# Kernel tuning notes

Measured on AMD Instinct MI355X. Metric: run time of the kernel, lower is better.

The kernel has to match this reference:

```python
import jax, jax.numpy as jnp
import numpy as np

N_NODES, N_EDGES, N_GRAPHS = 20000, 320000, 8
IN_CH, OUT_CH = 16, 64


def gat_conv(x, src, dst, W, a_src, a_dst, bias, heads, ch, concat):
    # PyG-style GATConv: linear -> per-edge attention logits -> edge softmax over dst -> scatter-sum
    n = x.shape[0]
    h = (x @ W).reshape(n, heads, ch)                      # [N,H,C]
    alpha_src = jnp.einsum('nhc,hc->nh', h, a_src)          # [N,H]
    alpha_dst = jnp.einsum('nhc,hc->nh', h, a_dst)
    e = jax.nn.leaky_relu(alpha_src[src] + alpha_dst[dst], 0.2)  # [E,H]
    emax = jax.ops.segment_max(e, dst, num_segments=n)      # safe: self-loops guarantee coverage
    ee = jnp.exp(e - emax[dst])
    denom = jax.ops.segment_sum(ee, dst, num_segments=n)
    alpha = ee / denom[dst]                                 # [E,H]
    msg = h[src] * alpha[:, :, None]                        # [E,H,C]
    out = jax.ops.segment_sum(msg, dst, num_segments=n)     # [N,H,C]
    out = out.reshape(n, heads * ch) if concat else out.mean(axis=1)
    return out + bias


def setup_inputs() -> dict:
    key = jax.random.key(0)
    ks = jax.random.split(key, 32)
    d = {}
    d['x'] = jax.random.normal(ks[0], (N_NODES, IN_CH), dtype=jnp.float32)
    d['edge_index'] = jax.random.randint(ks[1], (2, N_EDGES), 0, N_NODES)
    d['function_idx'] = jax.random.randint(ks[2], (8000,), 0, N_NODES)
    d['flag'] = jnp.sort(jax.random.randint(ks[3], (8000,), 0, N_GRAPHS))
    d['decision_var_idxes'] = jax.random.randint(ks[4], (N_GRAPHS,), 0, N_NODES)
    s = 0.1
    # conv1: in 16 -> 8 heads x 8
    d['W1'] = jax.random.normal(ks[5], (IN_CH, 64)) * s
    d['a_src1'] = jax.random.normal(ks[6], (8, 8)) * s
    d['a_dst1'] = jax.random.normal(ks[7], (8, 8)) * s
    d['b1'] = jnp.zeros((64,), jnp.float32)
    # conv2, conv3: 64 -> 8 heads x 8
    d['W2'] = jax.random.normal(ks[8], (64, 64)) * s
    d['a_src2'] = jax.random.normal(ks[9], (8, 8)) * s
    d['a_dst2'] = jax.random.normal(ks[10], (8, 8)) * s
    d['b2'] = jnp.zeros((64,), jnp.float32)
    d['W3'] = jax.random.normal(ks[11], (64, 64)) * s
    d['a_src3'] = jax.random.normal(ks[12], (8, 8)) * s
    d['a_dst3'] = jax.random.normal(ks[13], (8, 8)) * s
    d['b3'] = jnp.zeros((64,), jnp.float32)
    # conv4: 64 -> 4 heads x 64, concat=False (mean over heads)
    d['W4'] = jax.random.normal(ks[14], (64, 4 * OUT_CH)) * s
    d['a_src4'] = jax.random.normal(ks[15], (4, OUT_CH)) * s
    d['a_dst4'] = jax.random.normal(ks[16], (4, OUT_CH)) * s
    d['b4'] = jnp.zeros((OUT_CH,), jnp.float32)
    d['Wp'] = jax.random.normal(ks[17], (OUT_CH, OUT_CH)) * s
    d['Wt'] = jax.random.normal(ks[18], (OUT_CH, OUT_CH)) * s
    d['Wo'] = jax.random.normal(ks[19], (2 * OUT_CH, 1)) * s
    d['bo'] = jnp.zeros((1,), jnp.float32)
    return d


def reference(x, edge_index, function_idx, flag, decision_var_idxes,
              W1, a_src1, a_dst1, b1, W2, a_src2, a_dst2, b2,
              W3, a_src3, a_dst3, b3, W4, a_src4, a_dst4, b4,
              Wp, Wt, Wo, bo):
    n = x.shape[0]
    loops = jnp.arange(n)
    src = jnp.concatenate([edge_index[0], loops])
    dst = jnp.concatenate([edge_index[1], loops])
    h = jax.nn.elu(gat_conv(x, src, dst, W1, a_src1, a_dst1, b1, 8, 8, True))
    h = jax.nn.elu(gat_conv(h, src, dst, W2, a_src2, a_dst2, b2, 8, 8, True))
    h = jax.nn.elu(gat_conv(h, src, dst, W3, a_src3, a_dst3, b3, 8, 8, True))
    h = jax.nn.elu(gat_conv(h, src, dst, W4, a_src4, a_dst4, b4, 4, OUT_CH, False))
    # per-graph sum-pool over function nodes
    fp = jax.ops.segment_sum(h[function_idx], flag, num_segments=N_GRAPHS)  # [B,64]
    fp = fp @ Wp
    tgt = h[decision_var_idxes] @ Wt                                        # [B,64]
    z = jax.nn.elu(jnp.concatenate([fp, tgt], axis=1))                      # [B,128]
    return z @ Wo + bo                                                      # [B,1]
```

## Files before the change

kernel.cpp:

```cpp
#include <hip/hip_runtime.h>
#include <hip/hip_bf16.h>
#include <math.h>

typedef __hip_bfloat16 bf16;
typedef unsigned short u16;
typedef __attribute__((ext_vector_type(8))) short bf16x8;
typedef __attribute__((ext_vector_type(4))) float f32x4;

#define DEG_CAP 96

__device__ __forceinline__ float b2f(bf16 v){ return __bfloat162float(v); }
__device__ __forceinline__ u16 f2bu(float f){
  bf16 h = __float2bfloat16(f);
  return *reinterpret_cast<u16*>(&h);
}
__device__ __forceinline__ float bu2f(u16 u){
  bf16 h = *reinterpret_cast<bf16*>(&u);
  return __bfloat162float(h);
}
__device__ __forceinline__ float eluf(float x){ return x > 0.f ? x : __expf(x) - 1.f; }
__device__ __forceinline__ float lrelu(float x){ return x > 0.f ? x : 0.2f * x; }
__device__ __forceinline__ float ldr(const void* p, int i, int f){
  return f ? ((const float*)p)[i] : b2f(((const bf16*)p)[i]);
}

#define DPP_F(x, ctrl) __int_as_float(__builtin_amdgcn_update_dpp(0, __float_as_int(x), (ctrl), 0xF, 0xF, true))
__device__ __forceinline__ float dpp_max8(float x){
  x = fmaxf(x, DPP_F(x, 0xB1));
  x = fmaxf(x, DPP_F(x, 0x4E));
  x = fmaxf(x, DPP_F(x, 0x141));
  return x;
}
__device__ __forceinline__ float dpp_sum8(float x){
  x += DPP_F(x, 0xB1);
  x += DPP_F(x, 0x4E);
  x += DPP_F(x, 0x141);
  return x;
}
__device__ __forceinline__ float dpp_max16(float x){
  x = fmaxf(x, DPP_F(x, 0xB1));
  x = fmaxf(x, DPP_F(x, 0x4E));
  x = fmaxf(x, DPP_F(x, 0x141));
  x = fmaxf(x, DPP_F(x, 0x140));
  return x;
}
__device__ __forceinline__ float dpp_sum16(float x){
  x += DPP_F(x, 0xB1);
  x += DPP_F(x, 0x4E);
  x += DPP_F(x, 0x141);
  x += DPP_F(x, 0x140);
  return x;
}
__device__ __forceinline__ float dpp_addx1(float x){ return x + DPP_F(x, 0xB1); }

__global__ void detect_zero_k(const u16* __restrict__ x, int nprobe, int* __restrict__ flag,
                              int* __restrict__ fill, float* __restrict__ fp,
                              int* __restrict__ ticket, int n){
  int i = blockIdx.x * 256 + threadIdx.x;
  if (i < n) fill[i] = 0;
  if (i < 512) fp[i] = 0.f;
  if (i == 0) *ticket = 0;
  if (blockIdx.x == 0){
    __shared__ int bad_s;
    if (threadIdx.x == 0) bad_s = 0;
    __syncthreads();
    int bad = 0;
    for (int k = threadIdx.x; k < nprobe; k += 256){
      int ex = (x[k] >> 7) & 0xFF;
      if (ex >= 0xC6) bad = 1;
    }
    if (bad) atomicOr(&bad_s, 1);
    __syncthreads();
    if (threadIdx.x == 0) *flag = bad_s;
  }
}

struct ConvDesc {
  const void* src[17];
  int off[18];
};

__global__ void prep_k(ConvDesc d, float* __restrict__ out, const int* __restrict__ flag,
                       int total, const int* __restrict__ ei, int E, int n,
                       int* __restrict__ fill, int* __restrict__ esrc,
                       const void* __restrict__ W4r, const void* __restrict__ as4r,
                       const void* __restrict__ ad4r, float* __restrict__ avs,
                       float* __restrict__ avd, u16* __restrict__ wzh,
                       u16* __restrict__ wzl,
                       const void* __restrict__ x_raw, const void* __restrict__ W1r,
                       const void* __restrict__ as1r, const void* __restrict__ ad1r,
                       u16* __restrict__ hl1, float* __restrict__ asrc1,
                       float* __restrict__ adst1,
                       int CB, int EB){
  __shared__ float wl1[16 * 64];
  __shared__ float xr1[16][20];
  int b = blockIdx.x;
  int f = *flag;
  int t = threadIdx.x;
  if (b < CB){
    int i = b * 256 + t;
    if (i >= total) return;
    int a = 0;
    while (i >= d.off[a + 1]) ++a;
    out[i] = ldr(d.src[a], i - d.off[a], f);
  } else if (b < CB + EB){
    int e = (b - CB) * 256 + t;
    if (e >= E + n) return;
    int s, dd;
    if (e < E){ s = ei[e]; dd = ei[E + e]; } else { s = e - E; dd = s; }
    int pos = atomicAdd(&fill[dd], 1);
    if (pos < DEG_CAP) esrc[dd * DEG_CAP + pos] = s;
  } else if (b < CB + EB + 64){
    int pb = b - CB - EB;
    int g = pb * 256 + t;
    int r = g >> 6, c = g & 63;
    int h = r >> 6, k = r & 63;
    float ww = 0.25f * ldr(W4r, k * 256 + h * 64 + c, f);
    u16 hi = f2bu(ww);
    wzh[c * 256 + r] = hi;
    wzl[c * 256 + r] = f2bu(ww - bu2f(hi));
    if (pb == 0){
      int th = t >> 6, tk = t & 63;
      float s1 = 0.f, s2 = 0.f;
      for (int cc = 0; cc < 64; ++cc){
        float w = ldr(W4r, tk * 256 + th * 64 + cc, f);
        s1 += w * ldr(as4r, th * 64 + cc, f);
        s2 += w * ldr(ad4r, th * 64 + cc, f);
      }
      avs[t] = s1;
      avd[t] = s2;
    }
  } else {
    int lb = b - CB - EB - 64;
    int base = lb * 16;
    int lane = t & 63, wv = t >> 6;
    int node = wv * 4 + (lane >> 4);
    int jj = lane & 15;
    for (int i = t; i < 1024; i += 256) wl1[i] = ldr(W1r, i, f);
    for (int q = t; q < 64; q += 256){
      int nd = q >> 2, k4 = q & 3;
      float4 v = make_float4(0.f, 0.f, 0.f, 0.f);
      if (base + nd < n){
        if (f){
          v = *(const float4*)((const float*)x_raw + (base + nd) * 16 + k4 * 4);
        } else {
          ushort4 v4 = *(const ushort4*)((const u16*)x_raw + (base + nd) * 16 + k4 * 4);
          v = make_float4(bu2f(v4.x), bu2f(v4.y), bu2f(v4.z), bu2f(v4.w));
        }
      }
      *(float4*)(&xr1[nd][k4 * 4]) = v;
    }
    __syncthreads();
    float ax = 0.f, ay = 0.f, az = 0.f, aw = 0.f;
#pragma unroll
    for (int k4 = 0; k4 < 4; ++k4){
      float4 xv = *(const float4*)(&xr1[node][k4 * 4]);
      float4 w0 = ((const float4*)wl1)[(k4 * 4 + 0) * 16 + jj];
      float4 w1 = ((const float4*)wl1)[(k4 * 4 + 1) * 16 + jj];
      float4 w2 = ((const float4*)wl1)[(k4 * 4 + 2) * 16 + jj];
      float4 w3 = ((const float4*)wl1)[(k4 * 4 + 3) * 16 + jj];
      ax += xv.x * w0.x + xv.y * w1.x + xv.z * w2.x + xv.w * w3.x;
      ay += xv.x * w0.y + xv.y * w1.y + xv.z * w2.y + xv.w * w3.y;
      az += xv.x * w0.z + xv.y * w1.z + xv.z * w2.z + xv.w * w3.z;
      aw += xv.x * w0.w + xv.y * w1.w + xv.z * w2.w + xv.w * w3.w;
    }
    int gn = base + node;
    if (gn < n){
      ushort4 o4;
      o4.x = f2bu(ax); o4.y = f2bu(ay); o4.z = f2bu(az); o4.w = f2bu(aw);
      ((ushort4*)(hl1 + gn * 64))[jj] = o4;
    }
    float as_[4], ad_[4];
#pragma unroll
    for (int c = 0; c < 4; ++c){
      as_[c] = ldr(as1r, 4 * jj + c, f);
      ad_[c] = ldr(ad1r, 4 * jj + c, f);
    }
    float s1 = ax * as_[0] + ay * as_[1] + az * as_[2] + aw * as_[3];
    float s2 = ax * ad_[0] + ay * ad_[1] + az * ad_[2] + aw * ad_[3];
    s1 = dpp_addx1(s1);
    s2 = dpp_addx1(s2);
    if (gn < n){
      int hh = jj >> 1;
      if ((jj & 1) == 0) asrc1[gn * 8 + hh] = s1;
      else               adst1[gn * 8 + hh] = s2;
    }
  }
}

template<int NEXT>
__global__ void agg8f_k(const u16* __restrict__ hlin, const float* __restrict__ asrc,
                        const float* __restrict__ adst, const int* __restrict__ cnts,
                        const int* __restrict__ esrc, const float* __restrict__ bias,
                        const float* __restrict__ Wn,
                        const float* __restrict__ a_srcn, const float* __restrict__ a_dstn,
                        const float* __restrict__ avs, const float* __restrict__ avd,
                        u16* __restrict__ hout, u16* __restrict__ ylin,
                        float* __restrict__ asrco, float* __restrict__ adsto, int n){
  __shared__ float wl[NEXT == 1 ? 4096 : 1];
  __shared__ float os[4][64];
  if (NEXT == 1){
    for (int q = threadIdx.x; q < 1024; q += 256)
      ((float4*)wl)[q] = ((const float4*)Wn)[q];
    __syncthreads();
  }
  int node = (blockIdx.x * blockDim.x + threadIdx.x) >> 6;
  if (node >= n) return;
  int lane = threadIdx.x & 63;
  int wv = (threadIdx.x >> 6) & 3;
  int h = lane >> 3;
  int j = lane & 7;
  int cp = lane & 15;
  int q  = lane >> 4;
  int hh = cp >> 1;
  int wlane0 = hh * 8 + q;
  int wlane1 = hh * 8 + 4 + q;
  int sclane = hh * 8;
  int beg = node * DEG_CAP;
  int cnt = cnts[node]; if (cnt > DEG_CAP) cnt = DEG_CAP;
  int end = beg + cnt;
  float ad = adst[node * 8 + h];

  float m = -INFINITY, swp = 0.f;
  float4 acc = make_float4(0.f, 0.f, 0.f, 0.f);

  int   s_cur = 0; float l_cur = -INFINITY;
  if (beg + j < end){ s_cur = esrc[beg + j]; l_cur = lrelu(asrc[s_cur * 8 + h] + ad); }
  int s0c = __shfl(s_cur, q), s1c = __shfl(s_cur, 4 + q);
  ushort4 hv0 = *(const ushort4*)(hlin + s0c * 64 + cp * 4);
  ushort4 hv1 = *(const ushort4*)(hlin + s1c * 64 + cp * 4);
  int   s_nx = 0; float l_nx = -INFINITY;
  if (beg + 8 + j < end){ s_nx = esrc[beg + 8 + j]; l_nx = lrelu(asrc[s_nx * 8 + h] + ad); }

  for (int b0 = beg; b0 < end; b0 += 8){
    int s0n = __shfl(s_nx, q), s1n = __shfl(s_nx, 4 + q);
    ushort4 hv0n = *(const ushort4*)(hlin + s0n * 64 + cp * 4);
    ushort4 hv1n = *(const ushort4*)(hlin + s1n * 64 + cp * 4);
    int p2 = b0 + 16 + j;
    int s_n2 = 0; float l_n2 = -INFINITY;
    if (p2 < end){ s_n2 = esrc[p2]; l_n2 = lrelu(asrc[s_n2 * 8 + h] + ad); }
    float bm = dpp_max8(l_cur);
    float mn = fmaxf(m, bm);
    if (!__all(bm <= m)){
      float scale = __expf(m - mn);
      swp *= scale;
      float scale_g = __shfl(scale, sclane);
      acc.x *= scale_g; acc.y *= scale_g; acc.z *= scale_g; acc.w *= scale_g;
      m = mn;
    }
    float w = (b0 + j < end) ? __expf(l_cur - m) : 0.f;
    swp += w;
    float w0 = __shfl(w, wlane0);
    float w1 = __shfl(w, wlane1);
    acc.x += bu2f(hv0.x) * w0 + bu2f(hv1.x) * w1;
    acc.y += bu2f(hv0.y) * w0 + bu2f(hv1.y) * w1;
    acc.z += bu2f(hv0.z) * w0 + bu2f(hv1.z) * w1;
    acc.w += bu2f(hv0.w) * w0 + bu2f(hv1.w) * w1;
    hv0 = hv0n; hv1 = hv1n;
    l_cur = l_nx;
    s_nx = s_n2; l_nx = l_n2;
  }
  acc.x += __shfl_xor(acc.x, 16); acc.x += __shfl_xor(acc.x, 32);
  acc.y += __shfl_xor(acc.y, 16); acc.y += __shfl_xor(acc.y, 32);
  acc.z += __shfl_xor(acc.z, 16); acc.z += __shfl_xor(acc.z, 32);
  acc.w += __shfl_xor(acc.w, 16); acc.w += __shfl_xor(acc.w, 32);
  swp = dpp_sum8(swp);
  float sw_g = __shfl(swp, sclane);
  float4 bv = ((const float4*)bias)[cp];
  float4 o4;
  o4.x = eluf(acc.x / sw_g + bv.x);
  o4.y = eluf(acc.y / sw_g + bv.y);
  o4.z = eluf(acc.z / sw_g + bv.z);
  o4.w = eluf(acc.w / sw_g + bv.w);

  if (NEXT == 1){
    if (lane < 16) *(float4*)(&os[wv][cp * 4]) = o4;
    int jj = lane & 15, kk = lane >> 4;
    const float4* osr = (const float4*)(&os[wv][kk * 16]);
    float ax = 0.f, ay = 0.f, az = 0.f, aw = 0.f;
#pragma unroll
    for (int k4 = 0; k4 < 4; ++k4){
      float4 xv = osr[k4];
      float4 w0 = ((const float4*)wl)[(kk * 16 + k4 * 4 + 0) * 16 + jj];
      float4 w1 = ((const float4*)wl)[(kk * 16 + k4 * 4 + 1) * 16 + jj];
      float4 w2 = ((const float4*)wl)[(kk * 16 + k4 * 4 + 2) * 16 + jj];
      float4 w3 = ((const float4*)wl)[(kk * 16 + k4 * 4 + 3) * 16 + jj];
      ax += xv.x * w0.x + xv.y * w1.x + xv.z * w2.x + xv.w * w3.x;
      ay += xv.x * w0.y + xv.y * w1.y + xv.z * w2.y + xv.w * w3.y;
      az += xv.x * w0.z + xv.y * w1.z + xv.z * w2.z + xv.w * w3.z;
      aw += xv.x * w0.w + xv.y * w1.w + xv.z * w2.w + xv.w * w3.w;
    }
    ax += __shfl_xor(ax, 16); ax += __shfl_xor(ax, 32);
    ay += __shfl_xor(ay, 16); ay += __shfl_xor(ay, 32);
    az += __shfl_xor(az, 16); az += __shfl_xor(az, 32);
    aw += __shfl_xor(aw, 16); aw += __shfl_xor(aw, 32);
    if (lane < 16){
      ushort4 y4;
      y4.x = f2bu(ax); y4.y = f2bu(ay); y4.z = f2bu(az); y4.w = f2bu(aw);
      ((ushort4*)(ylin + node * 64))[jj] = y4;
      float4 as = *(const float4*)(a_srcn + 4 * jj);
      float4 adn = *(const float4*)(a_dstn + 4 * jj);
      float s1 = ax * as.x + ay * as.y + az * as.z + aw * as.w;
      float s2 = ax * adn.x + ay * adn.y + az * adn.z + aw * adn.w;
      s1 = dpp_addx1(s1);
      s2 = dpp_addx1(s2);
      int nh = jj >> 1;
      if ((jj & 1) == 0) asrco[node * 8 + nh] = s1;
      else               adsto[node * 8 + nh] = s2;
    }
  } else {
    if (lane < 16){
      ushort4 ho;
      ho.x = f2bu(o4.x); ho.y = f2bu(o4.y); ho.z = f2bu(o4.z); ho.w = f2bu(o4.w);
      ((ushort4*)(hout + node * 64))[cp] = ho;
      *(float4*)(&os[wv][cp * 4]) = o4;
    }
    int t8 = lane & 7, ah = (lane >> 3) & 3, sd = lane >> 5;
    const float* av = sd ? avd : avs;
    const float4* op = (const float4*)(&os[wv][t8 * 8]);
    const float4* ap = (const float4*)(av + ah * 64 + t8 * 8);
    float4 o0 = op[0], o1 = op[1];
    float4 a0 = ap[0], a1 = ap[1];
    float part = o0.x * a0.x + o0.y * a0.y + o0.z * a0.z + o0.w * a0.w
               + o1.x * a1.x + o1.y * a1.y + o1.z * a1.z + o1.w * a1.w;
    part = dpp_sum8(part);
    if (t8 == 0){
      if (sd == 0) asrco[node * 4 + ah] = part;
      else         adsto[node * 4 + ah] = part;
    }
  }
}

__global__ void aggz_k(const u16* __restrict__ h3, const float* __restrict__ asrc,
                       const float* __restrict__ adst, const int* __restrict__ cnts,
                       const int* __restrict__ esrc, u16* __restrict__ z, int n){
  int node = (blockIdx.x * blockDim.x + threadIdx.x) >> 6;
  if (node >= n) return;
  int lane = threadIdx.x & 63;
  int h = lane >> 4, j = lane & 15;
  int beg = node * DEG_CAP;
  int cnt = cnts[node]; if (cnt > DEG_CAP) cnt = DEG_CAP;
  int end = beg + cnt;
  float4 adv = *(const float4*)(adst + node * 4);
  float adh = h == 0 ? adv.x : h == 1 ? adv.y : h == 2 ? adv.z : adv.w;

  float m = -INFINITY, swp = 0.f;
  float acc[4][4] = {{0.f, 0.f, 0.f, 0.f}, {0.f, 0.f, 0.f, 0.f},
                     {0.f, 0.f, 0.f, 0.f}, {0.f, 0.f, 0.f, 0.f}};
  int   s_nx = 0; float l_nx = -INFINITY;
  if (beg + j < end){ s_nx = esrc[beg + j]; l_nx = lrelu(asrc[s_nx * 4 + h] + adh); }
  for (int b0 = beg; b0 < end; b0 += 16){
    int s = s_nx; float l = l_nx;
    int p2 = b0 + 16 + j;
    s_nx = 0; l_nx = -INFINITY;
    if (p2 < end){ s_nx = esrc[p2]; l_nx = lrelu(asrc[s_nx * 4 + h] + adh); }
    float bm = dpp_max16(l);
    float mn = fmaxf(m, bm);
    if (!__all(bm <= m)){
      float scale = __expf(m - mn);
      swp *= scale;
      float sc0 = __shfl(scale, 0),  sc1 = __shfl(scale, 16);
      float sc2 = __shfl(scale, 32), sc3 = __shfl(scale, 48);
#pragma unroll
      for (int c = 0; c < 4; ++c){
        acc[0][c] *= sc0; acc[1][c] *= sc1; acc[2][c] *= sc2; acc[3][c] *= sc3;
      }
      m = mn;
    }
    float w = (b0 + j < end) ? __expf(l - m) : 0.f;
    swp += w;
#pragma unroll
    for (int e4 = 0; e4 < 4; ++e4){
      int sl = e4 * 4 + h;
      int se = __shfl(s, sl);
      float w0 = __shfl(w, sl);
      float w1 = __shfl(w, 16 + sl);
      float w2 = __shfl(w, 32 + sl);
      float w3 = __shfl(w, 48 + sl);
      ushort4 hv = *(const ushort4*)(h3 + (size_t)se * 64 + j * 4);
      float x0 = bu2f(hv.x), x1 = bu2f(hv.y), x2 = bu2f(hv.z), x3 = bu2f(hv.w);
      acc[0][0] += x0 * w0; acc[0][1] += x1 * w0; acc[0][2] += x2 * w0; acc[0][3] += x3 * w0;
      acc[1][0] += x0 * w1; acc[1][1] += x1 * w1; acc[1][2] += x2 * w1; acc[1][3] += x3 * w1;
      acc[2][0] += x0 * w2; acc[2][1] += x1 * w2; acc[2][2] += x2 * w2; acc[2][3] += x3 * w2;
      acc[3][0] += x0 * w3; acc[3][1] += x1 * w3; acc[3][2] += x2 * w3; acc[3][3] += x3 * w3;
    }
  }
  swp = dpp_sum16(swp);
#pragma unroll
  for (int hh = 0; hh < 4; ++hh){
#pragma unroll
    for (int c = 0; c < 4; ++c){
      acc[hh][c] += __shfl_xor(acc[hh][c], 16);
      acc[hh][c] += __shfl_xor(acc[hh][c], 32);
    }
  }
  float swh = __shfl(swp, h * 16);
  float inv = 1.f / swh;
#pragma unroll
  for (int hh = 0; hh < 4; ++hh){
    if (h == hh){
      ushort4 o;
      o.x = f2bu(acc[hh][0] * inv); o.y = f2bu(acc[hh][1] * inv);
      o.z = f2bu(acc[hh][2] * inv); o.w = f2bu(acc[hh][3] * inv);
      ((ushort4*)(z + (size_t)node * 256))[hh * 16 + j] = o;
    }
  }
}

__global__ void linear4_mfma_k(const u16* __restrict__ Z, const u16* __restrict__ Wh,
                               const u16* __restrict__ Wl, const float* __restrict__ bias,
                               u16* __restrict__ H4, int n){
  int lane = threadIdx.x & 63;
  int wv = threadIdx.x >> 6;
  int base = blockIdx.x * 64 + wv * 16;
  if (base >= n) return;
  int r16 = lane & 15, kg = lane >> 4;
  int row = base + r16;
  int rowc = row < n ? row : n - 1;
  const u16* zp = Z + (size_t)rowc * 256 + kg * 8;
  const u16* wh = Wh + r16 * 256 + kg * 8;
  const u16* wlp = Wl + r16 * 256 + kg * 8;
  f32x4 ac[4] = {{0.f, 0.f, 0.f, 0.f}, {0.f, 0.f, 0.f, 0.f},
                 {0.f, 0.f, 0.f, 0.f}, {0.f, 0.f, 0.f, 0.f}};
#pragma unroll
  for (int k0 = 0; k0 < 256; k0 += 32){
    bf16x8 a = *(const bf16x8*)(zp + k0);
#pragma unroll
    for (int ct = 0; ct < 4; ++ct){
      bf16x8 bh = *(const bf16x8*)(wh + ct * 4096 + k0);
      ac[ct] = __builtin_amdgcn_mfma_f32_16x16x32_bf16(a, bh, ac[ct], 0, 0, 0);
    }
#pragma unroll
    for (int ct = 0; ct < 4; ++ct){
      bf16x8 bl = *(const bf16x8*)(wlp + ct * 4096 + k0);
      ac[ct] = __builtin_amdgcn_mfma_f32_16x16x32_bf16(a, bl, ac[ct], 0, 0, 0);
    }
  }
  int r0 = base + kg * 4;
#pragma unroll
  for (int ct = 0; ct < 4; ++ct){
    int jj = ct * 16 + r16;
    float bj = bias[jj];
#pragma unroll
    for (int i = 0; i < 4; ++i){
      int r = r0 + i;
      if (r < n) H4[(size_t)r * 64 + jj] = f2bu(eluf(ac[ct][i] + bj));
    }
  }
}

__global__ void pool_final_k(const u16* __restrict__ h, const int* __restrict__ fidx,
                             const int* __restrict__ flag_arr, float* __restrict__ fp,
                             int m, int* __restrict__ ticket, const int* __restrict__ dec,
                             const float* __restrict__ Wp, const float* __restrict__ Wt,
                             const float* __restrict__ Wo, const float* __restrict__ bo,
                             void* __restrict__ out, const int* __restrict__ dflag){
  __shared__ float acc[512];
  __shared__ int last_s;
  int t = threadIdx.x;
  for (int i = t; i < 512; i += 256) acc[i] = 0.f;
  __syncthreads();
  int lane = t & 63;
  int wave = (blockIdx.x * 256 + t) >> 6;
  int nwaves = (gridDim.x * 256) >> 6;
  for (int i = wave; i < m; i += nwaves){
    int g = flag_arr[i];
    int node = fidx[i];
    atomicAdd(&acc[g * 64 + lane], bu2f(h[node * 64 + lane]));
  }
  __syncthreads();
  for (int i = t; i < 512; i += 256) atomicAdd(&fp[i], acc[i]);
  __threadfence();
  if (t == 0) last_s = (atomicAdd(ticket, 1) == (int)gridDim.x - 1);
  __syncthreads();
  if (!last_s) return;
  __threadfence();
  volatile const float* fpv = fp;
  for (int gt = t; gt < 512; gt += 256){
    int g = gt >> 6, j = gt & 63;
    const u16* tr = h + dec[g] * 64;
    float a = 0.f, b = 0.f;
    for (int k = 0; k < 64; ++k){
      a += fpv[g * 64 + k] * Wp[k * 64 + j];
      b += bu2f(tr[k]) * Wt[k * 64 + j];
    }
    float v = eluf(a) * Wo[j] + eluf(b) * Wo[64 + j];
    for (int off = 32; off > 0; off >>= 1) v += __shfl_down(v, off);
    if (j == 0){
      float r = v + bo[0];
      if (*dflag) ((float*)out)[g] = r;
      else        ((bf16*)out)[g] = __float2bfloat16(r);
    }
  }
}


extern "C" void kernel_launch(void* const* d_in, const int* in_sizes, int n_in,
                              void* d_out, int out_size, void* d_ws, size_t ws_size,
                              hipStream_t stream) {
  const int*  ei    = (const int*)d_in[1];
  const int*  fidx  = (const int*)d_in[2];
  const int*  flagg = (const int*)d_in[3];
  const int*  dec   = (const int*)d_in[4];

  const int N = in_sizes[0] / 16;
  const int E = in_sizes[1] / 2;
  const int M = in_sizes[2];
  const int ET = E + N;

  const int fidxs[17] = {5,6,7,8,9,10,11,12,13,14,15,16,20,21,22,23,24};
  ConvDesc cd;
  int tot = 0;
  for (int k = 0; k < 17; ++k){
    cd.src[k] = d_in[fidxs[k]];
    cd.off[k] = tot;
    tot += in_sizes[fidxs[k]];
  }
  cd.off[17] = tot;

  char* p = (char*)d_ws;
  auto carve = [&](size_t bytes) -> void* {
    void* r = (void*)p;
    p += (bytes + 255) & ~(size_t)255;
    return r;
  };
  int*   dflag   = (int*)carve(4);
  int*   ticket  = (int*)carve(4);
  float* conv    = (float*)carve((size_t)tot * 4);
  u16*   hlA     = (u16*)carve((size_t)N * 64 * 2);
  u16*   hlB     = (u16*)carve((size_t)N * 64 * 2);
  u16*   h3buf   = (u16*)carve((size_t)N * 64 * 2);
  u16*   zbuf    = (u16*)carve((size_t)N * 256 * 2);
  u16*   h4buf   = (u16*)carve((size_t)N * 64 * 2);
  float* asrcA   = (float*)carve((size_t)N * 8 * 4);
  float* adstA   = (float*)carve((size_t)N * 8 * 4);
  float* asrcB   = (float*)carve((size_t)N * 8 * 4);
  float* adstB   = (float*)carve((size_t)N * 8 * 4);
  int*   fill    = (int*)carve((size_t)N * 4);
  int*   esrc    = (int*)carve((size_t)N * DEG_CAP * 4);
  float* fp      = (float*)carve(8 * 64 * 4);
  float* avs     = (float*)carve(256 * 4);
  float* avd     = (float*)carve(256 * 4);
  u16*   wzh     = (u16*)carve(16384 * 2);
  u16*   wzl     = (u16*)carve(16384 * 2);

  if ((size_t)(p - (char*)d_ws) > ws_size) return;

  const float* cas2 = conv + cd.off[5],  *cad2 = conv + cd.off[6],  *cb1 = conv + cd.off[3];
  const float* cW2 = conv + cd.off[4],   *cb2 = conv + cd.off[7];
  const float* cW3 = conv + cd.off[8],  *cas3 = conv + cd.off[9],  *cad3 = conv + cd.off[10], *cb3 = conv + cd.off[11];
  const float* cb4 = conv + cd.off[12];
  const float* cWp = conv + cd.off[13], *cWt = conv + cd.off[14], *cWo = conv + cd.off[15], *cbo = conv + cd.off[16];

  const int TB = 256;
  int nprobe = in_sizes[0] < 4096 ? in_sizes[0] : 4096;
  int zb_blocks = (N + 255) / 256;
  int CB = (tot + 255) / 256;
  int EB = (ET + 255) / 256;
  int ls_blocks = (N + 15) / 16;

  detect_zero_k<<<zb_blocks, TB, 0, stream>>>((const u16*)d_in[0], nprobe, dflag, fill, fp, ticket, N);
  prep_k<<<CB + EB + 64 + ls_blocks, TB, 0, stream>>>(
      cd, conv, dflag, tot, ei, E, N, fill, esrc,
      d_in[17], d_in[18], d_in[19], avs, avd, wzh, wzl,
      d_in[0], d_in[5], d_in[6], d_in[7], hlA, asrcA, adstA, CB, EB);

  int agg_blocks = (N * 64 + TB - 1) / TB;
  int mf_blocks  = (N + 63) / 64;

  agg8f_k<1><<<agg_blocks, TB, 0, stream>>>(hlA, asrcA, adstA, fill, esrc, cb1,
                                            cW2, cas2, cad2, nullptr, nullptr,
                                            nullptr, hlB, asrcB, adstB, N);
  agg8f_k<1><<<agg_blocks, TB, 0, stream>>>(hlB, asrcB, adstB, fill, esrc, cb2,
                                            cW3, cas3, cad3, nullptr, nullptr,
                                            nullptr, hlA, asrcA, adstA, N);
  agg8f_k<2><<<agg_blocks, TB, 0, stream>>>(hlA, asrcA, adstA, fill, esrc, cb3,
                                            nullptr, nullptr, nullptr, avs, avd,
                                            h3buf, nullptr, asrcB, adstB, N);
  aggz_k<<<agg_blocks, TB, 0, stream>>>(h3buf, asrcB, adstB, fill, esrc, zbuf, N);
  linear4_mfma_k<<<mf_blocks, TB, 0, stream>>>(zbuf, wzh, wzl, cb4, h4buf, N);
  pool_final_k<<<64, TB, 0, stream>>>(h4buf, fidx, flagg, fp, M, ticket, dec,
                                      cWp, cWt, cWo, cbo, d_out, dflag);
}
```

Before: 280.7 us.

## Chunk pool rows per block, prefetch gathers, and flush only touched graph slots

The pooling kernel now gives each block a contiguous chunk of the sorted function-index list and software-pipelines the index and feature loads two iterations ahead. Because flag is sorted, each block flushes only the graph slots in its own range and skips zero entries, which cuts global atomics. The grid grows from 64 to 256 blocks, and the last block copies the pooled sums into shared memory before the final matmul. The trade-off is more ticket atomics and more blocks for a small kernel that is a tiny part of total time.

Result: slower. 300.7 us (+7.1%).

```diff
diff --git a/kernel.cpp b/kernel.cpp
--- a/kernel.cpp
+++ b/kernel.cpp
@@ -458,30 +458,50 @@
   __shared__ float acc[512];
   __shared__ int last_s;
   int t = threadIdx.x;
+  int nb = gridDim.x;
+  int chunk = (m + nb - 1) / nb;
+  int beg = blockIdx.x * chunk;
+  int end = beg + chunk; if (end > m) end = m;
   for (int i = t; i < 512; i += 256) acc[i] = 0.f;
   __syncthreads();
   int lane = t & 63;
-  int wave = (blockIdx.x * 256 + t) >> 6;
-  int nwaves = (gridDim.x * 256) >> 6;
-  for (int i = wave; i < m; i += nwaves){
-    int g = flag_arr[i];
-    int node = fidx[i];
-    atomicAdd(&acc[g * 64 + lane], bu2f(h[node * 64 + lane]));
+  int wv = t >> 6;
+  int i0 = beg + wv;
+  int g0 = 0, n0 = 0;
+  if (i0 < end){ g0 = flag_arr[i0]; n0 = fidx[i0]; }
+  float hv0 = (i0 < end) ? bu2f(h[(size_t)n0 * 64 + lane]) : 0.f;
+  int g1 = 0, n1 = 0;
+  if (i0 + 4 < end){ g1 = flag_arr[i0 + 4]; n1 = fidx[i0 + 4]; }
+  for (int i = i0; i < end; i += 4){
+    float hv1 = (i + 4 < end) ? bu2f(h[(size_t)n1 * 64 + lane]) : 0.f;
+    int g2 = 0, n2 = 0;
+    if (i + 8 < end){ g2 = flag_arr[i + 8]; n2 = fidx[i + 8]; }
+    atomicAdd(&acc[g0 * 64 + lane], hv0);
+    hv0 = hv1; g0 = g1; n0 = n1; g1 = g2; n1 = n2;
   }
   __syncthreads();
-  for (int i = t; i < 512; i += 256) atomicAdd(&fp[i], acc[i]);
+  if (beg < end){
+    int gmin = flag_arr[beg], gmax = flag_arr[end - 1];
+    int cnt = (gmax - gmin + 1) * 64;
+    for (int i = t; i < cnt; i += 256){
+      float v = acc[gmin * 64 + i];
+      if (v != 0.f) atomicAdd(&fp[gmin * 64 + i], v);
+    }
+  }
   __threadfence();
-  if (t == 0) last_s = (atomicAdd(ticket, 1) == (int)gridDim.x - 1);
+  if (t == 0) last_s = (atomicAdd(ticket, 1) == nb - 1);
   __syncthreads();
   if (!last_s) return;
   __threadfence();
   volatile const float* fpv = fp;
+  for (int i = t; i < 512; i += 256) acc[i] = fpv[i];
+  __syncthreads();
   for (int gt = t; gt < 512; gt += 256){
     int g = gt >> 6, j = gt & 63;
-    const u16* tr = h + dec[g] * 64;
+    const u16* tr = h + (size_t)dec[g] * 64;
     float a = 0.f, b = 0.f;
     for (int k = 0; k < 64; ++k){
-      a += fpv[g * 64 + k] * Wp[k * 64 + j];
+      a += acc[g * 64 + k] * Wp[k * 64 + j];
       b += bu2f(tr[k]) * Wt[k * 64 + j];
     }
     float v = eluf(a) * Wo[j] + eluf(b) * Wo[64 + j];
@@ -579,6 +599,6 @@
                                             h3buf, nullptr, asrcB, adstB, N);
   aggz_k<<<agg_blocks, TB, 0, stream>>>(h3buf, asrcB, adstB, fill, esrc, zbuf, N);
   linear4_mfma_k<<<mf_blocks, TB, 0, stream>>>(zbuf, wzh, wzl, cb4, h4buf, N);
-  pool_final_k<<<64, TB, 0, stream>>>(h4buf, fidx, flagg, fp, M, ticket, dec,
-                                      cWp, cWt, cWo, cbo, d_out, dflag);
-}
+  pool_final_k<<<256, TB, 0, stream>>>(h4buf, fidx, flagg, fp, M, ticket, dec,
+                                       cWp, cWt, cWo, cbo, d_out, dflag);
+}
```
